# Kernel optimization log

Hardware: AMD Instinct MI355X
Metric: run time of the kernel (lower is better)

The kernel has to match this reference:

```python
import jax, jax.numpy as jnp
import numpy as np

TEMP = 0.05  # Trainer temp


def setup_inputs() -> dict:
    key = jax.random.key(0)
    k1, k2, k3 = jax.random.split(key, 3)
    B, C, D = 4096, 32768, 256
    x = jax.random.normal(k1, (B, D), dtype=jnp.float32)
    centrals = jax.random.normal(k2, (C, D), dtype=jnp.float32)
    # memory bank rows are kept unit-norm by the update rule
    centrals = centrals / jnp.linalg.norm(centrals, axis=1, keepdims=True)
    labels = jax.random.randint(k3, (B,), 0, C)
    return {"x": x, "centrals": centrals, "labels": labels}


def reference(x, centrals, labels):
    # new_f = F.normalize(model_out, dim=1)
    f = x / jnp.linalg.norm(x, axis=1, keepdims=True)          # [B, D]
    # CM.forward: inputs.mm(features.t()), then /= temp
    logits = (f @ centrals.T) / TEMP                           # [B, C]
    # ups = gather(exp(logits), labels); down = sum(exp(logits));  ups/down == softmax prob at label
    logp = jax.nn.log_softmax(logits, axis=1)
    p = jnp.exp(jnp.take_along_axis(logp, labels[:, None], axis=1)[:, 0])  # [B]
    return p
```

## Files before the change

### kernel.cpp

```cpp
#include <hip/hip_runtime.h>
#include <stdint.h>

typedef int i32x4 __attribute__((ext_vector_type(4)));
typedef int i32x8 __attribute__((ext_vector_type(8)));
typedef float f32x4 __attribute__((ext_vector_type(4)));

#define B_ROWS 4096
#define C_COLS 32768
#define D_DIM 256
#define LOG2E_OVER_TEMP 28.853900817779268f

#define BM 256
#define BC 64
#define CSPLIT 64
#define CPB (C_COLS / CSPLIT)
#define CTILES (CPB / BC)
#define NWAVES 4
#define TILE_BYTES (BC * D_DIM)
#define CVT_TILES (C_COLS / BC)

typedef __attribute__((address_space(3))) char lds_char_t;
typedef __attribute__((address_space(1))) const char glb_char_t;

__device__ __forceinline__ int pack4_fp8(float a, float b, float c, float d) {
  int r = 0;
  r = __builtin_amdgcn_cvt_pk_fp8_f32(a, b, r, false);
  r = __builtin_amdgcn_cvt_pk_fp8_f32(c, d, r, true);
  return r;
}

__global__ void prep_all(const float* __restrict__ x, const float* __restrict__ cent,
                         const int* __restrict__ labels, uint8_t* __restrict__ cq,
                         uint8_t* __restrict__ xq, float* __restrict__ elab) {
  int blk = blockIdx.x;
  if (blk < CVT_TILES) {
    int ct = blk;
    #pragma unroll
    for (int i = 0; i < 2; i++) {
      int s32 = i * 256 + threadIdx.x;
      int col = s32 >> 3;
      int j = s32 & 7;
      int k32 = j ^ (col & 7);
      const float* src = cent + (size_t)(ct * 64 + col) * D_DIM + k32 * 32;
      i32x4 o0, o1;
      #pragma unroll
      for (int q = 0; q < 4; q++) {
        float4 v = ((const float4*)src)[q];
        o0[q] = pack4_fp8(v.x, v.y, v.z, v.w);
      }
      #pragma unroll
      for (int q = 0; q < 4; q++) {
        float4 v = ((const float4*)src)[q + 4];
        o1[q] = pack4_fp8(v.x, v.y, v.z, v.w);
      }
      uint8_t* dst = cq + (size_t)ct * TILE_BYTES + s32 * 32;
      *(i32x4*)dst = o0;
      *(i32x4*)(dst + 16) = o1;
    }
  } else {
    int row = (blk - CVT_TILES) * (blockDim.x >> 6) + (threadIdx.x >> 6);
    int lane = threadIdx.x & 63;
    int lab = labels[row];
    const float4 xv = *(const float4*)(x + (size_t)row * D_DIM + lane * 4);
    const float4 cv = *(const float4*)(cent + (size_t)lab * D_DIM + lane * 4);
    float ss = xv.x * xv.x + xv.y * xv.y + xv.z * xv.z + xv.w * xv.w;
    float dc = xv.x * cv.x + xv.y * cv.y + xv.z * cv.z + xv.w * cv.w;
    #pragma unroll
    for (int m = 1; m < 64; m <<= 1) {
      ss += __shfl_xor(ss, m, 64);
      dc += __shfl_xor(dc, m, 64);
    }
    float inv = 1.0f / sqrtf(ss);
    float sc = inv * LOG2E_OVER_TEMP;
    *(int*)(xq + (size_t)row * D_DIM + lane * 4) =
        pack4_fp8(xv.x * sc, xv.y * sc, xv.z * sc, xv.w * sc);
    if (lane == 0) elab[row] = exp2f(dc * inv * LOG2E_OVER_TEMP);
  }
}

__device__ __forceinline__ void stage_tile(const uint8_t* __restrict__ src, char* buf,
                                           int w, int lane) {
  #pragma unroll
  for (int i = 0; i < 4; i++) {
    int slot_hi = i * NWAVES + w;
    __builtin_amdgcn_global_load_lds(
        (glb_char_t*)(const void*)(src + slot_hi * 1024 + lane * 16),
        (lds_char_t*)(void*)(buf + slot_hi * 1024), 16, 0, 0);
  }
}

__global__ void __launch_bounds__(256, 3)
gemm_expsum(const uint8_t* __restrict__ xq, const uint8_t* __restrict__ cq,
            float* __restrict__ partials) {
  __shared__ char Bs[2][TILE_BYTES];
  const int tid = threadIdx.x;
  const int w = tid >> 6, lane = tid & 63;
  const int fr = lane & 15, kq = lane >> 4;

  const int bid = blockIdx.x;
  const int xcd = bid & 7;
  const int j = bid >> 3;
  const int bx = j & 15;
  const int cs = xcd * 8 + (j >> 4);
  const int brow0 = bx * BM;
  const int tile0 = cs * CTILES;

  i32x8 a[4][2];
  #pragma unroll
  for (int rf = 0; rf < 4; rf++) {
    int row = brow0 + w * 64 + rf * 16 + fr;
    #pragma unroll
    for (int kh = 0; kh < 2; kh++)
      a[rf][kh] = *(const i32x8*)(xq + (size_t)row * D_DIM + kh * 128 + kq * 32);
  }

  float s[4][4] = {{0.f,0.f,0.f,0.f},{0.f,0.f,0.f,0.f},{0.f,0.f,0.f,0.f},{0.f,0.f,0.f,0.f}};
  const f32x4 vzero = {0.f, 0.f, 0.f, 0.f};

  stage_tile(cq + (size_t)tile0 * TILE_BYTES, Bs[0], w, lane);

  for (int t = 0; t < CTILES; t++) {
    __syncthreads();
    if (t + 1 < CTILES)
      stage_tile(cq + (size_t)(tile0 + t + 1) * TILE_BYTES, Bs[(t + 1) & 1], w, lane);

    const char* buf = Bs[t & 1];
    #pragma unroll
    for (int cf = 0; cf < 4; cf++) {
      const int col = cf * 16 + fr;
      i32x8 bf[2];
      #pragma unroll
      for (int kh = 0; kh < 2; kh++) {
        const int kbase = kh * 128 + kq * 32;
        const int off = col * 256 + (kbase ^ ((col & 7) << 5));
        bf[kh] = *(const i32x8*)(buf + off);
      }
      f32x4 acc[4];
      #pragma unroll
      for (int rf = 0; rf < 4; rf++) {
        acc[rf] = __builtin_amdgcn_mfma_scale_f32_16x16x128_f8f6f4(
            a[rf][0], bf[0], vzero, 0, 0, 0, 0x7F7F7F7F, 0, 0x7F7F7F7F);
        acc[rf] = __builtin_amdgcn_mfma_scale_f32_16x16x128_f8f6f4(
            a[rf][1], bf[1], acc[rf], 0, 0, 0, 0x7F7F7F7F, 0, 0x7F7F7F7F);
      }
      #pragma unroll
      for (int rf = 0; rf < 4; rf++)
        #pragma unroll
        for (int r = 0; r < 4; r++)
          s[rf][r] += __builtin_amdgcn_exp2f(acc[rf][r]);
    }
  }

  #pragma unroll
  for (int rf = 0; rf < 4; rf++)
    #pragma unroll
    for (int r = 0; r < 4; r++) {
      float v = s[rf][r];
      v += __shfl_xor(v, 1, 64);
      v += __shfl_xor(v, 2, 64);
      v += __shfl_xor(v, 4, 64);
      v += __shfl_xor(v, 8, 64);
      s[rf][r] = v;
    }
  if (fr == 0) {
    int rowbase = brow0 + w * 64;
    #pragma unroll
    for (int rf = 0; rf < 4; rf++)
      #pragma unroll
      for (int r = 0; r < 4; r++)
        partials[(size_t)cs * B_ROWS + rowbase + rf * 16 + kq * 4 + r] = s[rf][r];
  }
}

__global__ void finalize(const float* __restrict__ partials, const float* __restrict__ elab,
                         float* __restrict__ out) {
  int b = blockIdx.x * blockDim.x + threadIdx.x;
  if (b >= B_ROWS) return;
  float ssum = 0.f;
  #pragma unroll
  for (int cs = 0; cs < CSPLIT; cs++) ssum += partials[(size_t)cs * B_ROWS + b];
  out[b] = elab[b] / ssum;
}

extern "C" void kernel_launch(void* const* d_in, const int* in_sizes, int n_in,
                              void* d_out, int out_size, void* d_ws, size_t ws_size,
                              hipStream_t stream) {
  const float* x = (const float*)d_in[0];
  const float* cent = (const float*)d_in[1];
  const int* labels = (const int*)d_in[2];
  float* out = (float*)d_out;

  char* ws = (char*)d_ws;
  uint8_t* xq = (uint8_t*)ws;
  uint8_t* cq = (uint8_t*)(ws + (size_t)B_ROWS * D_DIM);
  float* partials = (float*)(ws + (size_t)B_ROWS * D_DIM + (size_t)C_COLS * D_DIM);
  float* elab = partials + (size_t)CSPLIT * B_ROWS;

  prep_all<<<CVT_TILES + B_ROWS / 4, 256, 0, stream>>>(x, cent, labels, cq, xq, elab);
  gemm_expsum<<<dim3(B_ROWS / BM * CSPLIT), 256, 0, stream>>>(xq, cq, partials);
  finalize<<<B_ROWS / 256, 256, 0, stream>>>(partials, elab, out);
}
```

Baseline: 84.07 us.

## Load B fragments directly from global in MFMA-native layout, dropping LDS staging

The centroid fp8 conversion now writes each 64-column tile in a k-chunk-major layout so that each lane's MFMA B fragment is a contiguous 32-byte run. The GEMM kernel then reads B fragments straight from global memory (L2/L1) instead of staging tiles through LDS with global_load_lds and double buffering, which also removes the per-tile __syncthreads. This trades LDS traffic and barrier stalls for more global/L1 load instructions per wave, and each wave now fetches B separately. Fully unrolling the tile loop raises register pressure and code size, and load latency is no longer hidden by a software pipeline.

Result: slower. 159.4 us (+89.6%).

```diff
diff --git a/kernel.cpp b/kernel.cpp
--- a/kernel.cpp
+++ b/kernel.cpp
@@ -15,12 +15,8 @@
 #define CSPLIT 64
 #define CPB (C_COLS / CSPLIT)
 #define CTILES (CPB / BC)
-#define NWAVES 4
 #define TILE_BYTES (BC * D_DIM)
 #define CVT_TILES (C_COLS / BC)
-
-typedef __attribute__((address_space(3))) char lds_char_t;
-typedef __attribute__((address_space(1))) const char glb_char_t;
 
 __device__ __forceinline__ int pack4_fp8(float a, float b, float c, float d) {
   int r = 0;
@@ -38,9 +34,8 @@
     #pragma unroll
     for (int i = 0; i < 2; i++) {
       int s32 = i * 256 + threadIdx.x;
-      int col = s32 >> 3;
-      int j = s32 & 7;
-      int k32 = j ^ (col & 7);
+      int col = s32 & 63;
+      int k32 = s32 >> 6;
       const float* src = cent + (size_t)(ct * 64 + col) * D_DIM + k32 * 32;
       i32x4 o0, o1;
       #pragma unroll
@@ -53,7 +48,7 @@
         float4 v = ((const float4*)src)[q + 4];
         o1[q] = pack4_fp8(v.x, v.y, v.z, v.w);
       }
-      uint8_t* dst = cq + (size_t)ct * TILE_BYTES + s32 * 32;
+      uint8_t* dst = cq + (size_t)ct * TILE_BYTES + k32 * 2048 + col * 32;
       *(i32x4*)dst = o0;
       *(i32x4*)(dst + 16) = o1;
     }
@@ -78,21 +73,9 @@
   }
 }
 
-__device__ __forceinline__ void stage_tile(const uint8_t* __restrict__ src, char* buf,
-                                           int w, int lane) {
-  #pragma unroll
-  for (int i = 0; i < 4; i++) {
-    int slot_hi = i * NWAVES + w;
-    __builtin_amdgcn_global_load_lds(
-        (glb_char_t*)(const void*)(src + slot_hi * 1024 + lane * 16),
-        (lds_char_t*)(void*)(buf + slot_hi * 1024), 16, 0, 0);
-  }
-}
-
 __global__ void __launch_bounds__(256, 3)
 gemm_expsum(const uint8_t* __restrict__ xq, const uint8_t* __restrict__ cq,
             float* __restrict__ partials) {
-  __shared__ char Bs[2][TILE_BYTES];
   const int tid = threadIdx.x;
   const int w = tid >> 6, lane = tid & 63;
   const int fr = lane & 15, kq = lane >> 4;
@@ -117,31 +100,30 @@
   float s[4][4] = {{0.f,0.f,0.f,0.f},{0.f,0.f,0.f,0.f},{0.f,0.f,0.f,0.f},{0.f,0.f,0.f,0.f}};
   const f32x4 vzero = {0.f, 0.f, 0.f, 0.f};
 
-  stage_tile(cq + (size_t)tile0 * TILE_BYTES, Bs[0], w, lane);
+  const uint8_t* bb = cq + (size_t)tile0 * TILE_BYTES + kq * 2048 + fr * 32;
 
+  #pragma unroll
   for (int t = 0; t < CTILES; t++) {
-    __syncthreads();
-    if (t + 1 < CTILES)
-      stage_tile(cq + (size_t)(tile0 + t + 1) * TILE_BYTES, Bs[(t + 1) & 1], w, lane);
-
-    const char* buf = Bs[t & 1];
     #pragma unroll
     for (int cf = 0; cf < 4; cf++) {
-      const int col = cf * 16 + fr;
-      i32x8 bf[2];
+      const uint8_t* p = bb + t * TILE_BYTES + cf * 512;
+      i32x4 bl0 = *(const i32x4*)(p);
+      i32x4 bh0 = *(const i32x4*)(p + 16);
+      i32x4 bl1 = *(const i32x4*)(p + 8192);
+      i32x4 bh1 = *(const i32x4*)(p + 8192 + 16);
+      i32x8 b0, b1;
       #pragma unroll
-      for (int kh = 0; kh < 2; kh++) {
-        const int kbase = kh * 128 + kq * 32;
-        const int off = col * 256 + (kbase ^ ((col & 7) << 5));
-        bf[kh] = *(const i32x8*)(buf + off);
+      for (int q = 0; q < 4; q++) {
+        b0[q] = bl0[q]; b0[q + 4] = bh0[q];
+        b1[q] = bl1[q]; b1[q + 4] = bh1[q];
       }
       f32x4 acc[4];
       #pragma unroll
       for (int rf = 0; rf < 4; rf++) {
         acc[rf] = __builtin_amdgcn_mfma_scale_f32_16x16x128_f8f6f4(
-            a[rf][0], bf[0], vzero, 0, 0, 0, 0x7F7F7F7F, 0, 0x7F7F7F7F);
+            a[rf][0], b0, vzero, 0, 0, 0, 0x7F7F7F7F, 0, 0x7F7F7F7F);
         acc[rf] = __builtin_amdgcn_mfma_scale_f32_16x16x128_f8f6f4(
-            a[rf][1], bf[1], acc[rf], 0, 0, 0, 0x7F7F7F7F, 0, 0x7F7F7F7F);
+            a[rf][1], b1, acc[rf], 0, 0, 0, 0x7F7F7F7F, 0, 0x7F7F7F7F);
       }
       #pragma unroll
       for (int rf = 0; rf < 4; rf++)
```
